# Kernel tuning notes

Measured on AMD Instinct MI355X. Metric: run time of the kernel, lower is better.

## Reference

```python
import jax, jax.numpy as jnp
import numpy as np

B = 2048        # batch
D_DENSE = 13    # dense input features
F = 7           # number of sparse features
CARD = 10000    # cardinality per sparse feature (== len(tokenizer_values))
E = 64          # embedding dim per feature
D_OUT = 32      # dense arch output size
S_OUT = 32      # sparse arch output size per feature
D_HID = 2 * D_OUT   # DenseArch MLP hidden (output_size*2 per code)
S_HID = 2 * S_OUT   # SparseArch MLP hidden (output_size*2 per code)
CONCAT = D_OUT + F * S_OUT    # 256
P_IN = CONCAT * CONCAT        # 65536, flattened outer product
P_HID = 512


def setup_inputs() -> dict:
    key = jax.random.key(0)
    ks = jax.random.split(key, 18)
    s = 0.05
    return {
        "dense_features": jax.random.normal(ks[0], (B, D_DENSE), dtype=jnp.float32),
        "sparse_features": jax.random.randint(ks[1], (B, F), 0, CARD, dtype=jnp.int64),
        # tokenizer_values per feature (shared arange, as in metadata)
        "tokenizers": jnp.arange(CARD, dtype=jnp.int64),
        # embedding tables stacked over features: [F, CARD, E]
        "emb_tables": jax.random.normal(ks[2], (F, CARD, E), dtype=jnp.float32) * s,
        # DenseArch MLP
        "dw1": jax.random.normal(ks[3], (D_DENSE, D_HID), dtype=jnp.float32) * s,
        "db1": jnp.zeros((D_HID,), dtype=jnp.float32),
        "dw2": jax.random.normal(ks[4], (D_HID, D_OUT), dtype=jnp.float32) * s,
        "db2": jnp.zeros((D_OUT,), dtype=jnp.float32),
        # per-feature sparse MLPs stacked over features
        "sw1": jax.random.normal(ks[5], (F, E, S_HID), dtype=jnp.float32) * s,
        "sb1": jnp.zeros((F, S_HID), dtype=jnp.float32),
        "sw2": jax.random.normal(ks[6], (F, S_HID, S_OUT), dtype=jnp.float32) * s,
        "sb2": jnp.zeros((F, S_OUT), dtype=jnp.float32),
        # PredictionLayer MLP
        "pw1": jax.random.normal(ks[7], (P_IN, P_HID), dtype=jnp.float32) * s,
        "pb1": jnp.zeros((P_HID,), dtype=jnp.float32),
        "pw2": jax.random.normal(ks[8], (P_HID, 1), dtype=jnp.float32) * s,
        "pb2": jnp.zeros((1,), dtype=jnp.float32),
    }


def reference(dense_features, sparse_features, tokenizers, emb_tables,
              dw1, db1, dw2, db2, sw1, sb1, sw2, sb2, pw1, pb1, pw2, pb2):
    # DenseArch: MLP(13 -> 64 -> 32)
    dense_out = jnp.maximum(dense_features @ dw1 + db1, 0.0) @ dw2 + db2  # [B, D_OUT]

    # SparseArch: equality-match argmax indexing (faithful to get_indices),
    # then embedding gather and per-feature MLP, vectorized over features.
    matches = sparse_features[:, :, None] == tokenizers[None, None, :]  # [B, F, CARD]
    idx = jnp.argmax(matches, axis=2)                                   # [B, F]
    gathered = emb_tables[jnp.arange(emb_tables.shape[0])[None, :], idx]  # [B, F, E]
    h = jnp.maximum(jnp.einsum('bfe,feh->bfh', gathered, sw1) + sb1, 0.0)
    sparse_out = jnp.einsum('bfh,fho->bfo', h, sw2) + sb2                # [B, F, S_OUT]

    # DenseSparseInteractionLayer: concat -> outer product -> flatten
    concat = jnp.concatenate(
        [dense_out, sparse_out.reshape(sparse_out.shape[0], -1)], axis=1)  # [B, CONCAT]
    outer = jnp.einsum('bi,bj->bij', concat, concat)
    flattened = outer.reshape(concat.shape[0], -1)                       # [B, CONCAT^2]

    # PredictionLayer: MLP(CONCAT^2 -> P_HID -> 1) + sigmoid, squeeze
    logits = jnp.maximum(flattened @ pw1 + pb1, 0.0) @ pw2 + pb2
    return jax.nn.sigmoid(logits).squeeze()
```

## Files before the change

### kernel.cpp

```cpp
#include <hip/hip_runtime.h>
#include <hip/hip_fp16.h>
#include <math.h>

#define BATCH 2048
#define NFEAT 7
#define CARD 10000
#define CONCAT 256
#define P_HID 512

#define BM 128
#define BN 128
#define BK 64
#define KSPLIT 16
#define NUNITS 640
#define TILES_PER_SPLIT 40
#define K_PAD (NUNITS * 64)
#define PREP_BLOCKS (NUNITS * 8)

using half8   = __attribute__((ext_vector_type(8))) _Float16;
using floatx4 = __attribute__((ext_vector_type(4))) float;

__device__ __forceinline__ void dma16(const _Float16* g, _Float16* l) {
    __builtin_amdgcn_global_load_lds(
        (const __attribute__((address_space(1))) unsigned int*)g,
        (__attribute__((address_space(3))) unsigned int*)l,
        16, 0, 0);
}

__device__ __forceinline__ void unit_decode(int u, int& i, int& jw) {
    if (u < 256)      { i = u;                jw = u >> 6; }
    else if (u < 448) { int v = u - 256; i = v / 3;        jw = 1 + v % 3; }
    else if (u < 576) { int v = u - 448; i = 64 + (v >> 1); jw = 2 + (v & 1); }
    else              { i = 128 + (u - 576); jw = 3; }
}

__global__ __launch_bounds__(256) void fused_pre(
    const float* __restrict__ dense, const int* __restrict__ sparse,
    const float* __restrict__ emb,
    const float* __restrict__ dw1, const float* __restrict__ db1,
    const float* __restrict__ dw2, const float* __restrict__ db2,
    const float* __restrict__ sw1, const float* __restrict__ sb1,
    const float* __restrict__ sw2, const float* __restrict__ sb2,
    const float* __restrict__ pw1,
    _Float16* __restrict__ cbf, _Float16* __restrict__ St)
{
    __shared__ float smem[64 * 65 + 8];
    const int tid = threadIdx.x;

    if (blockIdx.x < PREP_BLOCKS) {
        const int u = blockIdx.x >> 3, nc = blockIdx.x & 7;
        const int n0 = nc * 64;
        int i, jw;
        unit_decode(u, i, jw);

        const int c = tid & 15, qq = tid >> 4;
#pragma unroll
        for (int p = 0; p < 4; ++p) {
            const int q = qq + 16 * p;
            const int j = (jw << 6) + q;
            float4 s = {0.f, 0.f, 0.f, 0.f};
            if (j >= i) {
                s = *(const float4*)(pw1 + ((size_t)i * 256 + j) * P_HID + n0 + 4 * c);
                if (j > i) {
                    const float4 bv = *(const float4*)(pw1 + ((size_t)j * 256 + i) * P_HID + n0 + 4 * c);
                    s.x += bv.x; s.y += bv.y; s.z += bv.z; s.w += bv.w;
                }
            }
            float* dst = &smem[q * 65 + 4 * c];
            dst[0] = s.x; dst[1] = s.y; dst[2] = s.z; dst[3] = s.w;
        }
        __syncthreads();

        const int e = tid & 7, nn = tid >> 3;
#pragma unroll
        for (int p2 = 0; p2 < 2; ++p2) {
            const int n = nn + 32 * p2;
            half8 o;
#pragma unroll
            for (int q2 = 0; q2 < 8; ++q2)
                o[q2] = (_Float16)smem[(8 * e + q2) * 65 + n];
            *(half8*)(St + (size_t)(n0 + n) * K_PAD + (size_t)u * 64 + 8 * e) = o;
        }
    } else {
        const int wv = tid >> 6, t = tid & 63;
        const int b = (blockIdx.x - PREP_BLOCKS) * 4 + wv;
        float* xs   = smem + wv * 13;
        float* bufA = smem + 64  + wv * 64;
        float* bufB = smem + 320 + wv * 64;

        if (t < 13) xs[t] = dense[b * 13 + t];
        __syncthreads();

        float h = db1[t];
#pragma unroll
        for (int d = 0; d < 13; ++d) h += xs[d] * dw1[d * 64 + t];
        bufA[t] = fmaxf(h, 0.f);
        __syncthreads();

        if (t < 32) {
            float o = db2[t];
#pragma unroll
            for (int k = 0; k < 64; ++k) o += bufA[k] * dw2[k * 32 + t];
            cbf[b * 256 + t] = (_Float16)o;
        }

        for (int f = 0; f < NFEAT; ++f) {
            __syncthreads();
            const int idx = sparse[b * NFEAT + f];
            bufB[t] = emb[((size_t)(f * CARD + idx)) * 64 + t];
            __syncthreads();
            float s = sb1[f * 64 + t];
#pragma unroll
            for (int e = 0; e < 64; ++e) s += bufB[e] * sw1[(f * 64 + e) * 64 + t];
            bufA[t] = fmaxf(s, 0.f);
            __syncthreads();
            if (t < 32) {
                float o = sb2[f * 32 + t];
#pragma unroll
                for (int k = 0; k < 64; ++k) o += bufA[k] * sw2[(f * 64 + k) * 32 + t];
                cbf[b * 256 + 32 + f * 32 + t] = (_Float16)o;
            }
        }
    }
}

__global__ __launch_bounds__(256, 4) void bilinear_gemm(
    const _Float16* __restrict__ cbf, const _Float16* __restrict__ St,
    _Float16* __restrict__ hidpart)
{
    __shared__ _Float16 Al[BM][BK + 8];
    __shared__ _Float16 Bl[BN][BK];

    const int b = blockIdx.x;
    const int xcd = b & 7, slot = b >> 3;
    const int mt = slot & 15;
    const int slice = ((slot >> 4) << 3) | xcd;
    const int nt = slice & 3, ks = slice >> 2;
    const int m0 = mt * BM, n0 = nt * BN;
    const int t0 = ks * TILES_PER_SPLIT;

    const int tid = threadIdx.x, lane = tid & 63, wv = tid >> 6;
    const int wrow = (wv & 1) * 64, wcol = (wv >> 1) * 64;
    const int arow = tid >> 1, ajoff = (tid & 1) * 32;

    floatx4 acc[4][4];
#pragma unroll
    for (int i = 0; i < 4; ++i)
#pragma unroll
        for (int j = 0; j < 4; ++j) acc[i][j] = (floatx4){0.f, 0.f, 0.f, 0.f};

    const _Float16* crow = cbf + (m0 + arow) * 256;
    const int drow = wv * 32 + (lane >> 3);
    const int eswz = (lane & 7) ^ ((lane >> 3) & 7);
    const _Float16* bsrc = St + (size_t)(n0 + drow) * K_PAD + (size_t)t0 * 64 + eswz * 8;
    _Float16* bdst = &Bl[wv * 32][0];

    for (int it = 0; it < TILES_PER_SPLIT; ++it) {
#pragma unroll
        for (int p = 0; p < 4; ++p)
            dma16(bsrc + (size_t)(p * 8) * K_PAD, bdst + (p * 8) * BK);
        bsrc += BK;

        int ui, ujw;
        unit_decode(t0 + it, ui, ujw);
        const _Float16 ci = crow[ui];
        const half8 civ = {ci, ci, ci, ci, ci, ci, ci, ci};
        const _Float16* cj = crow + (ujw << 6) + ajoff;
#pragma unroll
        for (int x = 0; x < 32; x += 8) {
            half8 v = *(const half8*)(cj + x);
            *(half8*)&Al[arow][ajoff + x] = v * civ;
        }
        __syncthreads();

#pragma unroll
        for (int kk = 0; kk < BK; kk += 32) {
            half8 af[4], bfr[4];
#pragma unroll
            for (int i = 0; i < 4; ++i)
                af[i] = *(const half8*)&Al[wrow + i * 16 + (lane & 15)][kk + (lane >> 4) * 8];
#pragma unroll
            for (int j = 0; j < 4; ++j) {
                const int s = (((kk >> 3) + (lane >> 4)) ^ (lane & 7)) * 8;
                bfr[j] = *(const half8*)&Bl[wcol + j * 16 + (lane & 15)][s];
            }
#pragma unroll
            for (int i = 0; i < 4; ++i)
#pragma unroll
                for (int j = 0; j < 4; ++j)
                    acc[i][j] = __builtin_amdgcn_mfma_f32_16x16x32_f16(
                        af[i], bfr[j], acc[i][j], 0, 0, 0);
        }
        __syncthreads();
    }

    _Float16* outp = hidpart + (size_t)ks * BATCH * P_HID;
    const int r0 = m0 + wrow + (lane >> 4) * 4;
    const int c0 = n0 + wcol + (lane & 15);
#pragma unroll
    for (int i = 0; i < 4; ++i)
#pragma unroll
        for (int j = 0; j < 4; ++j)
#pragma unroll
            for (int r = 0; r < 4; ++r)
                outp[(size_t)(r0 + i * 16 + r) * P_HID + c0 + j * 16] =
                    (_Float16)acc[i][j][r];
}

__global__ void finalize(const _Float16* __restrict__ hidpart,
                         const float* __restrict__ pb1,
                         const float* __restrict__ pw2,
                         const float* __restrict__ pb2,
                         float* __restrict__ out)
{
    const int b = blockIdx.x, t = threadIdx.x;
    float accv = 0.f;
#pragma unroll
    for (int h = 0; h < 2; ++h) {
        const int n = t + h * 256;
        float v = 0.f;
#pragma unroll
        for (int s = 0; s < KSPLIT; ++s)
            v += (float)hidpart[(size_t)s * BATCH * P_HID + (size_t)b * P_HID + n];
        v += pb1[n];
        v = fmaxf(v, 0.f);
        accv += v * pw2[n];
    }
#pragma unroll
    for (int off = 32; off; off >>= 1) accv += __shfl_down(accv, off, 64);
    __shared__ float red[4];
    const int lane = t & 63, wv = t >> 6;
    if (lane == 0) red[wv] = accv;
    __syncthreads();
    if (t == 0) {
        const float s = red[0] + red[1] + red[2] + red[3] + pb2[0];
        out[b] = 1.f / (1.f + expf(-s));
    }
}

extern "C" void kernel_launch(void* const* d_in, const int* in_sizes, int n_in,
                              void* d_out, int out_size, void* d_ws, size_t ws_size,
                              hipStream_t stream)
{
    const float* dense  = (const float*)d_in[0];
    const int*   sparse = (const int*)d_in[1];
    const float* emb = (const float*)d_in[3];
    const float* dw1 = (const float*)d_in[4];
    const float* db1 = (const float*)d_in[5];
    const float* dw2 = (const float*)d_in[6];
    const float* db2 = (const float*)d_in[7];
    const float* sw1 = (const float*)d_in[8];
    const float* sb1 = (const float*)d_in[9];
    const float* sw2 = (const float*)d_in[10];
    const float* sb2 = (const float*)d_in[11];
    const float* pw1 = (const float*)d_in[12];
    const float* pb1 = (const float*)d_in[13];
    const float* pw2 = (const float*)d_in[14];
    const float* pb2 = (const float*)d_in[15];

    char* ws = (char*)d_ws;
    _Float16* cbf     = (_Float16*)ws;
    _Float16* St      = (_Float16*)(ws + (1 << 20));
    _Float16* hidpart = (_Float16*)(ws + (1 << 20) + ((size_t)40 << 20));

    fused_pre<<<PREP_BLOCKS + BATCH / 4, 256, 0, stream>>>(
        dense, sparse, emb, dw1, db1, dw2, db2, sw1, sb1, sw2, sb2, pw1,
        cbf, St);
    bilinear_gemm<<<16 * 4 * KSPLIT, 256, 0, stream>>>(cbf, St, hidpart);
    finalize<<<BATCH, 256, 0, stream>>>(hidpart, pb1, pw2, pb2, (float*)d_out);
}
```

Measured before the change: 376.6 us.

## Store folded weights unit-major and vectorize split-K finalize reduction

The prep kernel now gives each 64-row unit of the symmetric-folded pw1 a single block that covers all 512 outputs in two halves. It writes St in a unit-major layout (unit, n, 64), so each unit's slab is contiguous and the GEMM's B-tile DMA strides by 64 elements instead of the large K_PAD row stride. Finalize is rewritten to read 16-byte half8 vectors per wave over split slices and reduce through shared memory. The goal is better write and read coalescing and locality for the weight transform and the reduction, at the cost of fewer, heavier prep blocks and a 32KB LDS footprint.

Result: faster. 360.3 us (-4.3%).

```diff
diff --git a/kernel.cpp b/kernel.cpp
--- a/kernel.cpp
+++ b/kernel.cpp
@@ -14,9 +14,9 @@
 #define KSPLIT 16
 #define NUNITS 640
 #define TILES_PER_SPLIT 40
-#define K_PAD (NUNITS * 64)
-#define PREP_BLOCKS (NUNITS * 8)
-
+#define UNIT_ST (512 * 64)
+
+using f16x4   = __attribute__((ext_vector_type(4))) _Float16;
 using half8   = __attribute__((ext_vector_type(8))) _Float16;
 using floatx4 = __attribute__((ext_vector_type(4))) float;
 
@@ -44,46 +44,50 @@
     const float* __restrict__ pw1,
     _Float16* __restrict__ cbf, _Float16* __restrict__ St)
 {
-    __shared__ float smem[64 * 65 + 8];
+    __shared__ __align__(16) _Float16 sh[64 * 256];
     const int tid = threadIdx.x;
 
-    if (blockIdx.x < PREP_BLOCKS) {
-        const int u = blockIdx.x >> 3, nc = blockIdx.x & 7;
-        const int n0 = nc * 64;
+    if (blockIdx.x < NUNITS) {
+        const int u = blockIdx.x;
         int i, jw;
         unit_decode(u, i, jw);
 
-        const int c = tid & 15, qq = tid >> 4;
-#pragma unroll
-        for (int p = 0; p < 4; ++p) {
-            const int q = qq + 16 * p;
-            const int j = (jw << 6) + q;
-            float4 s = {0.f, 0.f, 0.f, 0.f};
-            if (j >= i) {
-                s = *(const float4*)(pw1 + ((size_t)i * 256 + j) * P_HID + n0 + 4 * c);
-                if (j > i) {
-                    const float4 bv = *(const float4*)(pw1 + ((size_t)j * 256 + i) * P_HID + n0 + 4 * c);
-                    s.x += bv.x; s.y += bv.y; s.z += bv.z; s.w += bv.w;
+        for (int nh = 0; nh < 2; ++nh) {
+            const int nb = nh * 256;
+            if (nh) __syncthreads();
+
+#pragma unroll
+            for (int m = 0; m < 16; ++m) {
+                const int flat = m * 256 + tid;
+                const int q = flat >> 6, c4 = flat & 63;
+                const int j = (jw << 6) + q;
+                float4 s = {0.f, 0.f, 0.f, 0.f};
+                if (j >= i) {
+                    s = *(const float4*)(pw1 + ((size_t)i * 256 + j) * P_HID + nb + 4 * c4);
+                    if (j > i) {
+                        const float4 mv = *(const float4*)(pw1 + ((size_t)j * 256 + i) * P_HID + nb + 4 * c4);
+                        s.x += mv.x; s.y += mv.y; s.z += mv.z; s.w += mv.w;
+                    }
                 }
-            }
-            float* dst = &smem[q * 65 + 4 * c];
-            dst[0] = s.x; dst[1] = s.y; dst[2] = s.z; dst[3] = s.w;
-        }
-        __syncthreads();
-
-        const int e = tid & 7, nn = tid >> 3;
-#pragma unroll
-        for (int p2 = 0; p2 < 2; ++p2) {
-            const int n = nn + 32 * p2;
-            half8 o;
-#pragma unroll
-            for (int q2 = 0; q2 < 8; ++q2)
-                o[q2] = (_Float16)smem[(8 * e + q2) * 65 + n];
-            *(half8*)(St + (size_t)(n0 + n) * K_PAD + (size_t)u * 64 + 8 * e) = o;
+                f16x4 hv = {(_Float16)s.x, (_Float16)s.y, (_Float16)s.z, (_Float16)s.w};
+                *(f16x4*)(sh + q * 256 + 4 * c4) = hv;
+            }
+            __syncthreads();
+
+            const _Float16* col = sh + tid;
+            _Float16* outp = St + (size_t)u * UNIT_ST + (size_t)(nb + tid) * 64;
+#pragma unroll
+            for (int e = 0; e < 8; ++e) {
+                half8 o;
+#pragma unroll
+                for (int r = 0; r < 8; ++r) o[r] = col[(8 * e + r) * 256];
+                *(half8*)(outp + 8 * e) = o;
+            }
         }
     } else {
+        float* smem = (float*)sh;
         const int wv = tid >> 6, t = tid & 63;
-        const int b = (blockIdx.x - PREP_BLOCKS) * 4 + wv;
+        const int b = (blockIdx.x - NUNITS) * 4 + wv;
         float* xs   = smem + wv * 13;
         float* bufA = smem + 64  + wv * 64;
         float* bufB = smem + 320 + wv * 64;
@@ -152,14 +156,14 @@
     const _Float16* crow = cbf + (m0 + arow) * 256;
     const int drow = wv * 32 + (lane >> 3);
     const int eswz = (lane & 7) ^ ((lane >> 3) & 7);
-    const _Float16* bsrc = St + (size_t)(n0 + drow) * K_PAD + (size_t)t0 * 64 + eswz * 8;
+    const _Float16* bsrc = St + (size_t)t0 * UNIT_ST + (size_t)(n0 + drow) * 64 + eswz * 8;
     _Float16* bdst = &Bl[wv * 32][0];
 
     for (int it = 0; it < TILES_PER_SPLIT; ++it) {
 #pragma unroll
         for (int p = 0; p < 4; ++p)
-            dma16(bsrc + (size_t)(p * 8) * K_PAD, bdst + (p * 8) * BK);
-        bsrc += BK;
+            dma16(bsrc + (size_t)(p * 8) * 64, bdst + (p * 8) * BK);
+        bsrc += UNIT_ST;
 
         int ui, ujw;
         unit_decode(t0 + it, ui, ujw);
@@ -207,34 +211,51 @@
                     (_Float16)acc[i][j][r];
 }
 
-__global__ void finalize(const _Float16* __restrict__ hidpart,
-                         const float* __restrict__ pb1,
-                         const float* __restrict__ pw2,
-                         const float* __restrict__ pb2,
-                         float* __restrict__ out)
+__global__ __launch_bounds__(256) void finalize(
+    const _Float16* __restrict__ hidpart,
+    const float* __restrict__ pb1,
+    const float* __restrict__ pw2,
+    const float* __restrict__ pb2,
+    float* __restrict__ out)
 {
     const int b = blockIdx.x, t = threadIdx.x;
-    float accv = 0.f;
-#pragma unroll
-    for (int h = 0; h < 2; ++h) {
-        const int n = t + h * 256;
-        float v = 0.f;
-#pragma unroll
-        for (int s = 0; s < KSPLIT; ++s)
-            v += (float)hidpart[(size_t)s * BATCH * P_HID + (size_t)b * P_HID + n];
-        v += pb1[n];
-        v = fmaxf(v, 0.f);
-        accv += v * pw2[n];
-    }
-#pragma unroll
-    for (int off = 32; off; off >>= 1) accv += __shfl_down(accv, off, 64);
-    __shared__ float red[4];
-    const int lane = t & 63, wv = t >> 6;
-    if (lane == 0) red[wv] = accv;
+    const int wv = t >> 6, lane = t & 63;
+
+    float acc[8];
+#pragma unroll
+    for (int k = 0; k < 8; ++k) acc[k] = 0.f;
+
+#pragma unroll
+    for (int si = 0; si < 4; ++si) {
+        const int s = wv + 4 * si;
+        const half8 v = *(const half8*)(hidpart + (size_t)s * BATCH * P_HID
+                                        + (size_t)b * P_HID + lane * 8);
+#pragma unroll
+        for (int k = 0; k < 8; ++k) acc[k] += (float)v[k];
+    }
+
+    __shared__ float red[4 * 512];
+#pragma unroll
+    for (int k = 0; k < 8; ++k) red[wv * 512 + k * 64 + lane] = acc[k];
     __syncthreads();
-    if (t == 0) {
-        const float s = red[0] + red[1] + red[2] + red[3] + pb2[0];
-        out[b] = 1.f / (1.f + expf(-s));
+
+    if (wv == 0) {
+        float dot = 0.f;
+#pragma unroll
+        for (int k = 0; k < 8; ++k) {
+            const int n = lane * 8 + k;
+            float v = red[k * 64 + lane] + red[512 + k * 64 + lane]
+                    + red[1024 + k * 64 + lane] + red[1536 + k * 64 + lane];
+            v += pb1[n];
+            v = fmaxf(v, 0.f);
+            dot += v * pw2[n];
+        }
+#pragma unroll
+        for (int off = 32; off; off >>= 1) dot += __shfl_down(dot, off, 64);
+        if (lane == 0) {
+            const float s = dot + pb2[0];
+            out[b] = 1.f / (1.f + expf(-s));
+        }
     }
 }
 
@@ -263,7 +284,7 @@
     _Float16* St      = (_Float16*)(ws + (1 << 20));
     _Float16* hidpart = (_Float16*)(ws + (1 << 20) + ((size_t)40 << 20));
 
-    fused_pre<<<PREP_BLOCKS + BATCH / 4, 256, 0, stream>>>(
+    fused_pre<<<NUNITS + BATCH / 4, 256, 0, stream>>>(
         dense, sparse, emb, dw1, db1, dw2, db2, sw1, sb1, sw2, sb2, pw1,
         cbf, St);
     bilinear_gemm<<<16 * 4 * KSPLIT, 256, 0, stream>>>(cbf, St, hidpart);
```
